# Kernel tuning notes

Hardware: AMD Instinct MI355X
Metric: run time of the kernel (lower is better)

The kernel has to match this reference:

```python
import jax, jax.numpy as jnp
from jax import lax
import numpy as np

B, L, OBS_DIM, ACT_DIM = 4, 1024, 60, 2
D_MODEL, N_LAYERS, D_STATE, D_CONV, EXPAND = 256, 4, 16, 4, 2
D_INNER = EXPAND * D_MODEL
DT_RANK = (D_MODEL + 15) // 16  # mamba_ssm default: ceil(d_model/16)


def setup_inputs() -> dict:
    key = jax.random.key(0)
    ks = jax.random.split(key, 12)
    rn = lambda k, s, sc: jax.random.normal(k, s, jnp.float32) * sc
    return {
        "obs_seq": jax.random.normal(ks[0], (B, L, OBS_DIM), jnp.float32),
        "input_proj_w": rn(ks[1], (D_MODEL, OBS_DIM), OBS_DIM ** -0.5),
        "input_proj_b": jnp.zeros((D_MODEL,), jnp.float32),
        "norm_w": jnp.ones((N_LAYERS, D_MODEL), jnp.float32),
        "norm_b": jnp.zeros((N_LAYERS, D_MODEL), jnp.float32),
        "in_proj_w": rn(ks[2], (N_LAYERS, 2 * D_INNER, D_MODEL), D_MODEL ** -0.5),
        "conv_w": rn(ks[3], (N_LAYERS, D_INNER, D_CONV), D_CONV ** -0.5),
        "conv_b": jnp.zeros((N_LAYERS, D_INNER), jnp.float32),
        "x_proj_w": rn(ks[4], (N_LAYERS, DT_RANK + 2 * D_STATE, D_INNER), D_INNER ** -0.5),
        "dt_proj_w": rn(ks[5], (N_LAYERS, D_INNER, DT_RANK), DT_RANK ** -0.5),
        "dt_proj_b": jnp.full((N_LAYERS, D_INNER), float(np.log(np.expm1(0.01))), jnp.float32),
        "A_log": jnp.log(jnp.broadcast_to(jnp.arange(1, D_STATE + 1, dtype=jnp.float32), (N_LAYERS, D_INNER, D_STATE))),
        "D_skip": jnp.ones((N_LAYERS, D_INNER), jnp.float32),
        "out_proj_w": rn(ks[6], (N_LAYERS, D_MODEL, D_INNER), D_INNER ** -0.5),
        "policy_mean_w": rn(ks[7], (ACT_DIM, D_MODEL), 0.01 * D_MODEL ** -0.5),
        "policy_mean_b": jnp.zeros((ACT_DIM,), jnp.float32),
        "policy_log_std": jnp.zeros((ACT_DIM,), jnp.float32),
        "value_w": rn(ks[8], (1, D_MODEL), D_MODEL ** -0.5),
        "value_b": jnp.zeros((1,), jnp.float32),
    }


def _silu(x):
    return x * jax.nn.sigmoid(x)


def _layer_norm(x, w, b):
    m = jnp.mean(x, -1, keepdims=True)
    v = jnp.mean(jnp.square(x - m), -1, keepdims=True)
    return (x - m) * lax.rsqrt(v + 1e-5) * w + b


def _mamba(x, in_w, cw, cb, xw, dtw, dtb, a_log, d_skip, ow):
    # x: (B, L, d_model)
    xz = jnp.einsum('bld,ed->ble', x, in_w)            # (B, L, 2*d_inner)
    xi, z = xz[..., :D_INNER], xz[..., D_INNER:]
    # depthwise causal conv, width D_CONV
    xp = jnp.pad(xi, ((0, 0), (D_CONV - 1, 0), (0, 0)))
    conv = sum(xp[:, k:k + L, :] * cw[:, k] for k in range(D_CONV)) + cb
    xi = _silu(conv)
    dbc = jnp.einsum('bld,ed->ble', xi, xw)            # (B, L, dt_rank + 2*d_state)
    dt = jax.nn.softplus(jnp.einsum('blr,dr->bld', dbc[..., :DT_RANK], dtw) + dtb)
    Bm = dbc[..., DT_RANK:DT_RANK + D_STATE]           # (B, L, N)
    Cm = dbc[..., DT_RANK + D_STATE:]                  # (B, L, N)
    A = -jnp.exp(a_log)                                # (d_inner, N)
    dA = jnp.exp(dt[..., None] * A)                    # (B, L, d_inner, N)
    dBx = (dt * xi)[..., None] * Bm[:, :, None, :]     # (B, L, d_inner, N)

    def comb(c1, c2):
        a1, b1 = c1
        a2, b2 = c2
        return a2 * a1, a2 * b1 + b2

    _, h = lax.associative_scan(comb, (dA, dBx), axis=1)  # h_t = dA_t*h_{t-1} + dBx_t
    y = jnp.einsum('bldn,bln->bld', h, Cm) + d_skip * xi
    return jnp.einsum('bld,ed->ble', y * _silu(z), ow)


def _forward(obs_seq, input_proj_w, input_proj_b, norm_w, norm_b, in_proj_w, conv_w,
             conv_b, x_proj_w, dt_proj_w, dt_proj_b, A_log, D_skip, out_proj_w,
             policy_mean_w, policy_mean_b, policy_log_std, value_w, value_b):
    x = _silu(jnp.einsum('blo,do->bld', obs_seq, input_proj_w) + input_proj_b)
    for i in range(N_LAYERS):  # pre-norm residual Mamba blocks
        x = x + _mamba(_layer_norm(x, norm_w[i], norm_b[i]), in_proj_w[i], conv_w[i],
                       conv_b[i], x_proj_w[i], dt_proj_w[i], dt_proj_b[i], A_log[i],
                       D_skip[i], out_proj_w[i])
    mu = jnp.einsum('bld,ad->bla', x, policy_mean_w) + policy_mean_b
    std = jnp.broadcast_to(jnp.exp(policy_log_std), mu.shape)
    value = jnp.einsum('bld,od->blo', x, value_w) + value_b
    return mu, std, value


def reference(obs_seq, input_proj_w, input_proj_b, norm_w, norm_b, in_proj_w, conv_w,
              conv_b, x_proj_w, dt_proj_w, dt_proj_b, A_log, D_skip, out_proj_w,
              policy_mean_w, policy_mean_b, policy_log_std, value_w, value_b):
    return _forward(obs_seq, input_proj_w, input_proj_b, norm_w, norm_b, in_proj_w,
                    conv_w, conv_b, x_proj_w, dt_proj_w, dt_proj_b, A_log, D_skip,
                    out_proj_w, policy_mean_w, policy_mean_b, policy_log_std,
                    value_w, value_b)
```

## Files before the change

kernel.cpp:

```cpp
#include <hip/hip_runtime.h>
#include <hip/hip_bf16.h>

#define Bsz 4
#define Lseq 1024
#define OBS 60
#define DM 256
#define DI 512
#define DTR 16
#define DST 16
#define NTOK (Bsz*Lseq)
#define NCH 128
#define CH  8

typedef _Float16 half8 __attribute__((ext_vector_type(8)));
typedef float floatx4 __attribute__((ext_vector_type(4)));

__device__ __forceinline__ float silu_f(float v) {
    return v * (1.f / (1.f + __expf(-v)));
}
__device__ __forceinline__ float softplus_f(float v) {
    return fmaxf(v, 0.f) + log1pf(__expf(-fabsf(v)));
}

__device__ __forceinline__ void compute_dA(float dtv, const float* An,
                                           bool structured, float* dA) {
    if (structured) {
        float p1 = __expf(-dtv);
        float p2 = p1*p1, p4 = p2*p2, p8 = p4*p4;
        dA[0]=p1;      dA[1]=p2;      dA[2]=p2*p1;    dA[3]=p4;
        dA[4]=p4*p1;   dA[5]=p4*p2;   dA[6]=p4*dA[2]; dA[7]=p8;
        dA[8]=p8*p1;   dA[9]=p8*p2;   dA[10]=p8*dA[2];dA[11]=p8*p4;
        dA[12]=p8*dA[4];dA[13]=p8*dA[5];dA[14]=p8*dA[6];dA[15]=p8*p8;
    } else {
        #pragma unroll
        for (int n = 0; n < 16; ++n) dA[n] = __expf(dtv*An[n]);
    }
}

#define NIN_W  (4*1024*256)
#define NX_W   (4*64*512)
#define NOUT_W (4*256*512)
#define NCWT   (4*4*512)
#define NW_TOT (NIN_W + NX_W + NOUT_W + NCWT)
#define NWB    ((NW_TOT + 255)/256)
__global__ __launch_bounds__(256) void prep_kernel(
    const float* __restrict__ inw, const float* __restrict__ xw,
    const float* __restrict__ ow, const float* __restrict__ cw,
    _Float16* __restrict__ wh_in, _Float16* __restrict__ wh_x,
    _Float16* __restrict__ wh_out, _Float16* __restrict__ cwT,
    const float* __restrict__ obs, const float* __restrict__ ipw,
    const float* __restrict__ ipb, const float* __restrict__ nw,
    const float* __restrict__ nb, float* __restrict__ x,
    _Float16* __restrict__ xn_h) {
    __shared__ float so[OBS];
    __shared__ float ps[4];
    __shared__ float mean_s, rstd_s;
    int tid = threadIdx.x;
    if (blockIdx.x < NWB) {
        int idx = blockIdx.x*256 + tid;
        if (idx < NIN_W) {
            wh_in[idx] = (_Float16)inw[idx];
        } else if (idx < NIN_W + NX_W) {
            int r = idx - NIN_W;
            int layer = r >> 15;
            int rem = r & 32767;
            int n = rem >> 9, k = rem & 511;
            wh_x[r] = (_Float16)((n < 48) ? xw[((size_t)layer*48 + n)*512 + k] : 0.f);
        } else if (idx < NIN_W + NX_W + NOUT_W) {
            int r = idx - NIN_W - NX_W;
            wh_out[r] = (_Float16)ow[r];
        } else if (idx < NW_TOT) {
            int r = idx - NIN_W - NX_W - NOUT_W;
            int layer = r >> 11;
            int rem = r & 2047;
            int k = rem >> 9, d = rem & 511;
            cwT[r] = (_Float16)cw[layer*2048 + d*4 + k];
        }
        return;
    }
    int t = blockIdx.x - NWB;
    if (tid < OBS) so[tid] = obs[t*OBS + tid];
    __syncthreads();
    float acc = ipb[tid];
    const float* wr = ipw + tid*OBS;
    #pragma unroll
    for (int k = 0; k < OBS; ++k) acc += so[k]*wr[k];
    float v = silu_f(acc);
    x[t*DM + tid] = v;
    float s = v;
    #pragma unroll
    for (int off = 32; off; off >>= 1) s += __shfl_down(s, off);
    int wid = tid >> 6, lane = tid & 63;
    if (lane == 0) ps[wid] = s;
    __syncthreads();
    if (tid == 0) mean_s = (ps[0]+ps[1]+ps[2]+ps[3]) * (1.f/DM);
    __syncthreads();
    float m = mean_s;
    float d = v - m;
    float sq = d*d;
    #pragma unroll
    for (int off = 32; off; off >>= 1) sq += __shfl_down(sq, off);
    if (lane == 0) ps[wid] = sq;
    __syncthreads();
    if (tid == 0) rstd_s = rsqrtf((ps[0]+ps[1]+ps[2]+ps[3])*(1.f/DM) + 1e-5f);
    __syncthreads();
    xn_h[t*DM + tid] = (_Float16)(d * rstd_s * nw[tid] + nb[tid]);
}

template<int BM, int BN, int WM, int WN, int EPI>
__global__ __launch_bounds__(256) void hgemm_nt(
    const _Float16* __restrict__ A, const _Float16* __restrict__ W,
    void* __restrict__ Cout, const float* __restrict__ resid,
    int M, int N, int K, int ldc,
    const float* __restrict__ e0, const float* __restrict__ e1,
    const float* __restrict__ e2, const float* __restrict__ e3,
    const float* __restrict__ e4,
    float* __restrict__ xout, _Float16* __restrict__ xnh) {
    constexpr int MFR = BM/(WM*16);
    constexpr int NFR = BN/(WN*16);
    __shared__ _Float16 As[BM*64];
    __shared__ _Float16 Bs[BN*64];
    int tid = threadIdx.x;
    int r0 = blockIdx.y*BM, c0 = blockIdx.x*BN;
    int w = tid >> 6, lane = tid & 63;
    int wr = w / WN, wc = w % WN;
    floatx4 acc[MFR][NFR];
    #pragma unroll
    for (int i = 0; i < MFR; ++i)
        #pragma unroll
        for (int j = 0; j < NFR; ++j)
            acc[i][j] = (floatx4)0.f;

    for (int k0 = 0; k0 < K; k0 += 64) {
        #pragma unroll
        for (int c = 0; c < BM/32; ++c) {
            int q = tid + 256*c;
            int row = q >> 3, cc = (q & 7)*8;
            half8 v = *(const half8*)&A[(size_t)(r0 + row)*K + k0 + cc];
            *(half8*)&As[row*64 + (cc ^ ((row & 7) << 3))] = v;
        }
        #pragma unroll
        for (int c = 0; c < BN/32; ++c) {
            int q = tid + 256*c;
            int row = q >> 3, cc = (q & 7)*8;
            half8 v = *(const half8*)&W[(size_t)(c0 + row)*K + k0 + cc];
            *(half8*)&Bs[row*64 + (cc ^ ((row & 7) << 3))] = v;
        }
        __syncthreads();
        #pragma unroll
        for (int kc = 0; kc < 2; ++kc) {
            half8 a[MFR], b[NFR];
            int col = kc*32 + (lane >> 4)*8;
            #pragma unroll
            for (int i = 0; i < MFR; ++i) {
                int row = wr*(BM/WM) + i*16 + (lane & 15);
                a[i] = *(const half8*)&As[row*64 + (col ^ ((row & 7) << 3))];
            }
            #pragma unroll
            for (int j = 0; j < NFR; ++j) {
                int row = wc*(BN/WN) + j*16 + (lane & 15);
                b[j] = *(const half8*)&Bs[row*64 + (col ^ ((row & 7) << 3))];
            }
            #pragma unroll
            for (int i = 0; i < MFR; ++i)
                #pragma unroll
                for (int j = 0; j < NFR; ++j)
                    acc[i][j] = __builtin_amdgcn_mfma_f32_16x16x32_f16(a[i], b[j], acc[i][j], 0, 0, 0);
        }
        __syncthreads();
    }
    if constexpr (EPI == 1) {
        _Float16* C = (_Float16*)Cout;
        #pragma unroll
        for (int i = 0; i < MFR; ++i) {
            int m0 = r0 + wr*(BM/WM) + i*16 + (lane >> 4)*4;
            #pragma unroll
            for (int j = 0; j < NFR; ++j) {
                int col = c0 + wc*(BN/WN) + j*16 + (lane & 15);
                #pragma unroll
                for (int t = 0; t < 4; ++t)
                    C[(size_t)(m0 + t)*ldc + col] = (_Float16)acc[i][j][t];
            }
        }
    } else if constexpr (EPI == 2 || EPI == 3) {
        int g = lane >> 4, ln16 = lane & 15;
        #pragma unroll
        for (int t = 0; t < 4; ++t) {
            int row = r0 + wr*16 + g*4 + t;
            #pragma unroll
            for (int j = 0; j < NFR; ++j)
                acc[0][j][t] += resid[(size_t)row*DM + j*16 + ln16];
        }
        if constexpr (EPI == 2) {
            #pragma unroll
            for (int t = 0; t < 4; ++t) {
                int row = r0 + wr*16 + g*4 + t;
                float s = 0.f, sq = 0.f;
                #pragma unroll
                for (int j = 0; j < NFR; ++j) {
                    float v = acc[0][j][t];
                    xout[(size_t)row*DM + j*16 + ln16] = v;
                    s += v; sq += v*v;
                }
                #pragma unroll
                for (int msk = 1; msk < 16; msk <<= 1) {
                    s += __shfl_xor(s, msk);
                    sq += __shfl_xor(sq, msk);
                }
                float mean = s * (1.f/DM);
                float rstd = rsqrtf(sq*(1.f/DM) - mean*mean + 1e-5f);
                #pragma unroll
                for (int j = 0; j < NFR; ++j) {
                    int col = j*16 + ln16;
                    float v = acc[0][j][t];
                    xnh[(size_t)row*DM + col] =
                        (_Float16)((v - mean)*rstd*e0[col] + e1[col]);
                }
            }
        } else {
            float* out = xout;
            #pragma unroll
            for (int t = 0; t < 4; ++t) {
                int row = r0 + wr*16 + g*4 + t;
                float m0 = 0.f, m1 = 0.f, vv = 0.f;
                #pragma unroll
                for (int j = 0; j < NFR; ++j) {
                    int col = j*16 + ln16;
                    float v = acc[0][j][t];
                    m0 += v*e0[col]; m1 += v*e0[DM + col]; vv += v*e3[col];
                }
                #pragma unroll
                for (int msk = 1; msk < 16; msk <<= 1) {
                    m0 += __shfl_xor(m0, msk);
                    m1 += __shfl_xor(m1, msk);
                    vv += __shfl_xor(vv, msk);
                }
                if (ln16 == 0) {
                    out[row*2 + 0] = m0 + e1[0];
                    out[row*2 + 1] = m1 + e1[1];
                    out[2*NTOK + row*2 + 0] = __expf(e2[0]);
                    out[2*NTOK + row*2 + 1] = __expf(e2[1]);
                    out[4*NTOK + row] = vv + e4[0];
                }
            }
        }
    }
}

__global__ __launch_bounds__(256) void xproj_conv_gemm(
    const _Float16* __restrict__ xz_h, const _Float16* __restrict__ Wx,
    const _Float16* __restrict__ cwT, const float* __restrict__ cb,
    float* __restrict__ dbc) {
    __shared__ _Float16 As[32*64];
    __shared__ _Float16 Bs[64*64];
    int tid = threadIdx.x;
    int r0 = blockIdx.x*32;
    int w = tid >> 6, lane = tid & 63;
    int wr = w >> 1, wc = w & 1;
    floatx4 acc[2];
    acc[0] = (floatx4)0.f; acc[1] = (floatx4)0.f;
    for (int k0 = 0; k0 < 512; k0 += 64) {
        {
            int row = tid >> 3, e8 = tid & 7;
            int d = k0 + e8*8;
            int t = r0 + row, l = t & (Lseq-1);
            half8 zero8 = (half8)((_Float16)0.f);
            half8 v0 = (l >= 3) ? *(const half8*)&xz_h[(size_t)(t-3)*1024 + d] : zero8;
            half8 v1 = (l >= 2) ? *(const half8*)&xz_h[(size_t)(t-2)*1024 + d] : zero8;
            half8 v2 = (l >= 1) ? *(const half8*)&xz_h[(size_t)(t-1)*1024 + d] : zero8;
            half8 v3 = *(const half8*)&xz_h[(size_t)t*1024 + d];
            half8 c0 = *(const half8*)&cwT[0*512 + d];
            half8 c1 = *(const half8*)&cwT[1*512 + d];
            half8 c2 = *(const half8*)&cwT[2*512 + d];
            half8 c3 = *(const half8*)&cwT[3*512 + d];
            half8 o;
            #pragma unroll
            for (int e = 0; e < 8; ++e) {
                float a = cb[d + e];
                a += (float)v0[e]*(float)c0[e];
                a += (float)v1[e]*(float)c1[e];
                a += (float)v2[e]*(float)c2[e];
                a += (float)v3[e]*(float)c3[e];
                o[e] = (_Float16)silu_f(a);
            }
            *(half8*)&As[row*64 + ((e8*8) ^ ((row & 7) << 3))] = o;
        }
        #pragma unroll
        for (int c = 0; c < 2; ++c) {
            int q = tid + 256*c;
            int row = q >> 3, cc = (q & 7)*8;
            half8 vv = *(const half8*)&Wx[(size_t)row*512 + k0 + cc];
            *(half8*)&Bs[row*64 + (cc ^ ((row & 7) << 3))] = vv;
        }
        __syncthreads();
        #pragma unroll
        for (int kc = 0; kc < 2; ++kc) {
            int col = kc*32 + (lane >> 4)*8;
            int arow = wr*16 + (lane & 15);
            half8 a = *(const half8*)&As[arow*64 + (col ^ ((arow & 7) << 3))];
            #pragma unroll
            for (int j = 0; j < 2; ++j) {
                int brow = wc*32 + j*16 + (lane & 15);
                half8 b = *(const half8*)&Bs[brow*64 + (col ^ ((brow & 7) << 3))];
                acc[j] = __builtin_amdgcn_mfma_f32_16x16x32_f16(a, b, acc[j], 0, 0, 0);
            }
        }
        __syncthreads();
    }
    int m0 = r0 + wr*16 + (lane >> 4)*4;
    #pragma unroll
    for (int j = 0; j < 2; ++j) {
        int col = wc*32 + j*16 + (lane & 15);
        if (col < 48) {
            #pragma unroll
            for (int t = 0; t < 4; ++t)
                dbc[(size_t)(m0 + t)*48 + col] = acc[j][t];
        }
    }
}

__global__ __launch_bounds__(256) void scan_phaseA(
    const _Float16* __restrict__ xz_h, const float* __restrict__ dbc,
    const float* __restrict__ dtw, const float* __restrict__ dtb,
    const float* __restrict__ a_log, const float* __restrict__ cw,
    const float* __restrict__ cb,
    _Float16* __restrict__ xi_h, _Float16* __restrict__ dt_h,
    _Float16* __restrict__ Ap, _Float16* __restrict__ He) {
    __shared__ float sdbc[CH*48];
    int blk = blockIdx.x;
    int b = blk >> 8; int rem = blk & 255; int c = rem >> 1; int half = rem & 1;
    int d = half*256 + threadIdx.x;
    const float* src = dbc + ((size_t)(b*Lseq + c*CH))*48;
    for (int q = threadIdx.x; q < CH*48; q += 256) sdbc[q] = src[q];
    float wreg[16];
    #pragma unroll
    for (int r = 0; r < DTR; ++r) wreg[r] = dtw[d*DTR + r];
    float bias = dtb[d];
    float4 cwv = *(const float4*)&cw[d*4];
    float cbv = cb[d];
    float An[16];
    bool structured = true;
    #pragma unroll
    for (int n = 0; n < 16; ++n) {
        An[n] = -__expf(a_log[d*16 + n]);
        structured = structured && (fabsf(An[n] + (float)(n+1)) < 1e-4f*(n+1));
    }
    int l0 = c*CH; int t0 = b*Lseq + l0;
    float w0 = 0.f, w1 = 0.f, w2 = 0.f;
    if (l0 >= 3) {
        w0 = (float)xz_h[(size_t)(t0-3)*1024 + d];
        w1 = (float)xz_h[(size_t)(t0-2)*1024 + d];
        w2 = (float)xz_h[(size_t)(t0-1)*1024 + d];
    }
    __syncthreads();
    float h[16] = {};
    float ap[16];
    #pragma unroll
    for (int n = 0; n < 16; ++n) ap[n] = 1.f;
    #pragma unroll 4
    for (int s = 0; s < CH; ++s) {
        float cur = (float)xz_h[(size_t)(t0+s)*1024 + d];
        float conv = cbv + cwv.x*w0 + cwv.y*w1 + cwv.z*w2 + cwv.w*cur;
        w0 = w1; w1 = w2; w2 = cur;
        float xiv = silu_f(conv);
        float dl = bias;
        #pragma unroll
        for (int r = 0; r < DTR; ++r) dl += sdbc[s*48 + r]*wreg[r];
        float dtv = softplus_f(dl);
        size_t ti = (size_t)(t0+s)*DI + d;
        xi_h[ti] = (_Float16)xiv;
        dt_h[ti] = (_Float16)dtv;
        float u = dtv*xiv;
        float dA[16];
        compute_dA(dtv, An, structured, dA);
        #pragma unroll
        for (int n = 0; n < 16; ++n) {
            h[n] = dA[n]*h[n] + u*sdbc[s*48 + DTR + n];
            ap[n] *= dA[n];
        }
    }
    size_t base = ((size_t)(b*NCH + c)*16)*DI + d;
    #pragma unroll
    for (int n = 0; n < 16; ++n) {
        Ap[base + n*DI] = (_Float16)ap[n];
        He[base + n*DI] = (_Float16)h[n];
    }
}

__global__ __launch_bounds__(256) void scan_phaseB(
    const _Float16* __restrict__ Ap, const _Float16* __restrict__ He,
    _Float16* __restrict__ h0) {
    int g = blockIdx.x*blockDim.x + threadIdx.x;
    int b = g >> 13; int n = (g >> 9) & 15; int d = g & 511;
    float run = 0.f;
    for (int c = 0; c < NCH; ++c) {
        size_t idx = ((size_t)(b*NCH + c)*16 + n)*DI + d;
        float a = (float)Ap[idx], e = (float)He[idx];
        h0[idx] = (_Float16)run;
        run = a*run + e;
    }
}

__global__ __launch_bounds__(256) void scan_phaseC(
    const _Float16* __restrict__ xi_h, const _Float16* __restrict__ dt_h,
    const float* __restrict__ dbc, const float* __restrict__ a_log,
    const float* __restrict__ dskip, const _Float16* __restrict__ xz_h,
    const _Float16* __restrict__ h0, _Float16* __restrict__ yg_h) {
    __shared__ float sdbc[CH*48];
    int blk = blockIdx.x;
    int b = blk >> 8; int rem = blk & 255; int c = rem >> 1; int half = rem & 1;
    int d = half*256 + threadIdx.x;
    const float* src = dbc + ((size_t)(b*Lseq + c*CH))*48;
    for (int q = threadIdx.x; q < CH*48; q += 256) sdbc[q] = src[q];
    float An[16];
    bool structured = true;
    #pragma unroll
    for (int n = 0; n < 16; ++n) {
        An[n] = -__expf(a_log[d*16 + n]);
        structured = structured && (fabsf(An[n] + (float)(n+1)) < 1e-4f*(n+1));
    }
    __syncthreads();
    int t0 = b*Lseq + c*CH;
    float h[16];
    size_t base = ((size_t)(b*NCH + c)*16)*DI + d;
    #pragma unroll
    for (int n = 0; n < 16; ++n) h[n] = (float)h0[base + n*DI];
    float ds = dskip[d];
    #pragma unroll 4
    for (int s = 0; s < CH; ++s) {
        size_t ti = (size_t)(t0+s)*DI + d;
        float xiv = (float)xi_h[ti];
        float dtv = (float)dt_h[ti];
        float u = dtv*xiv;
        float dA[16];
        compute_dA(dtv, An, structured, dA);
        float y = ds*xiv;
        #pragma unroll
        for (int n = 0; n < 16; ++n) {
            h[n] = dA[n]*h[n] + u*sdbc[s*48 + DTR + n];
            y += h[n]*sdbc[s*48 + DTR + DST + n];
        }
        float zv = (float)xz_h[(size_t)(t0+s)*1024 + DI + d];
        yg_h[ti] = (_Float16)(y * silu_f(zv));
    }
}

extern "C" void kernel_launch(void* const* d_in, const int* in_sizes, int n_in,
                              void* d_out, int out_size, void* d_ws, size_t ws_size,
                              hipStream_t stream) {
    const float* obs = (const float*)d_in[0];
    const float* ipw = (const float*)d_in[1];
    const float* ipb = (const float*)d_in[2];
    const float* nw  = (const float*)d_in[3];
    const float* nb  = (const float*)d_in[4];
    const float* inw = (const float*)d_in[5];
    const float* cw  = (const float*)d_in[6];
    const float* cb  = (const float*)d_in[7];
    const float* xw  = (const float*)d_in[8];
    const float* dtw = (const float*)d_in[9];
    const float* dtb = (const float*)d_in[10];
    const float* alog= (const float*)d_in[11];
    const float* dsk = (const float*)d_in[12];
    const float* ow  = (const float*)d_in[13];
    const float* pw  = (const float*)d_in[14];
    const float* pb  = (const float*)d_in[15];
    const float* ls  = (const float*)d_in[16];
    const float* vw  = (const float*)d_in[17];
    const float* vb  = (const float*)d_in[18];
    float* out = (float*)d_out;

    float* ws = (float*)d_ws;
    float* x   = ws;
    float* dbc = x   + 1048576;
    _Float16* f16b  = (_Float16*)(dbc + 196608);
    _Float16* xz_h  = f16b;
    _Float16* xn_h  = xz_h  + 4194304;
    _Float16* xi_h  = xn_h  + 1048576;
    _Float16* dt_h  = xi_h  + 2097152;
    _Float16* yg_h  = dt_h  + 2097152;
    _Float16* Ap_h  = yg_h  + 2097152;
    _Float16* He_h  = Ap_h  + 4194304;
    _Float16* h0_h  = Ap_h;
    _Float16* wh_in = He_h  + 4194304;
    _Float16* wh_x  = wh_in + 1048576;
    _Float16* wh_out= wh_x  + 131072;
    _Float16* cwT_h = wh_out+ 524288;

    prep_kernel<<<NWB + NTOK, 256, 0, stream>>>(
        inw, xw, ow, cw, wh_in, wh_x, wh_out, cwT_h,
        obs, ipw, ipb, nw, nb, x, xn_h);

    for (int i = 0; i < 4; ++i) {
        {
            dim3 g(1024/64, NTOK/128);
            hgemm_nt<128,64,2,2,1><<<g, 256, 0, stream>>>(
                xn_h, wh_in + (size_t)i*1024*256, xz_h, nullptr, NTOK, 1024, 256, 1024,
                nullptr, nullptr, nullptr, nullptr, nullptr, nullptr, nullptr);
        }
        xproj_conv_gemm<<<NTOK/32, 256, 0, stream>>>(
            xz_h, wh_x + (size_t)i*64*512, cwT_h + i*2048, cb + i*DI, dbc);
        scan_phaseA<<<Bsz*NCH*2, 256, 0, stream>>>(
            xz_h, dbc, dtw + (size_t)i*DI*DTR, dtb + i*DI,
            alog + (size_t)i*DI*DST, cw + (size_t)i*DI*4, cb + i*DI,
            xi_h, dt_h, Ap_h, He_h);
        scan_phaseB<<<128, 256, 0, stream>>>(Ap_h, He_h, h0_h);
        scan_phaseC<<<Bsz*NCH*2, 256, 0, stream>>>(
            xi_h, dt_h, dbc, alog + (size_t)i*DI*DST,
            dsk + i*DI, xz_h, h0_h, yg_h);
        {
            dim3 g(1, NTOK/64);
            if (i < 3) {
                hgemm_nt<64,256,4,1,2><<<g, 256, 0, stream>>>(
                    yg_h, wh_out + (size_t)i*256*512, nullptr, x, NTOK, 256, 512, 256,
                    nw + (i+1)*DM, nb + (i+1)*DM, nullptr, nullptr, nullptr, x, xn_h);
            } else {
                hgemm_nt<64,256,4,1,3><<<g, 256, 0, stream>>>(
                    yg_h, wh_out + (size_t)i*256*512, nullptr, x, NTOK, 256, 512, 256,
                    pw, pb, ls, vw, vb, out, nullptr);
            }
        }
    }
}
```

Baseline: 337.3 us.

## Recompute dt in scan phase C and double the scan chunk length

```diff
diff --git a/kernel.cpp b/kernel.cpp
--- a/kernel.cpp
+++ b/kernel.cpp
@@ -9,8 +9,8 @@
 #define DTR 16
 #define DST 16
 #define NTOK (Bsz*Lseq)
-#define NCH 128
-#define CH  8
+#define NCH 64
+#define CH  16
 
 typedef _Float16 half8 __attribute__((ext_vector_type(8)));
 typedef float floatx4 __attribute__((ext_vector_type(4)));
@@ -324,11 +324,11 @@
     const float* __restrict__ dtw, const float* __restrict__ dtb,
     const float* __restrict__ a_log, const float* __restrict__ cw,
     const float* __restrict__ cb,
-    _Float16* __restrict__ xi_h, _Float16* __restrict__ dt_h,
+    _Float16* __restrict__ xi_h,
     _Float16* __restrict__ Ap, _Float16* __restrict__ He) {
     __shared__ float sdbc[CH*48];
     int blk = blockIdx.x;
-    int b = blk >> 8; int rem = blk & 255; int c = rem >> 1; int half = rem & 1;
+    int b = blk >> 7; int rem = blk & 127; int c = rem >> 1; int half = rem & 1;
     int d = half*256 + threadIdx.x;
     const float* src = dbc + ((size_t)(b*Lseq + c*CH))*48;
     for (int q = threadIdx.x; q < CH*48; q += 256) sdbc[q] = src[q];
@@ -357,7 +357,6 @@
     float ap[16];
     #pragma unroll
     for (int n = 0; n < 16; ++n) ap[n] = 1.f;
-    #pragma unroll 4
     for (int s = 0; s < CH; ++s) {
         float cur = (float)xz_h[(size_t)(t0+s)*1024 + d];
         float conv = cbv + cwv.x*w0 + cwv.y*w1 + cwv.z*w2 + cwv.w*cur;
@@ -367,9 +366,7 @@
         #pragma unroll
         for (int r = 0; r < DTR; ++r) dl += sdbc[s*48 + r]*wreg[r];
         float dtv = softplus_f(dl);
-        size_t ti = (size_t)(t0+s)*DI + d;
-        xi_h[ti] = (_Float16)xiv;
-        dt_h[ti] = (_Float16)dtv;
+        xi_h[(size_t)(t0+s)*DI + d] = (_Float16)xiv;
         float u = dtv*xiv;
         float dA[16];
         compute_dA(dtv, An, structured, dA);
@@ -402,16 +399,21 @@
 }
 
 __global__ __launch_bounds__(256) void scan_phaseC(
-    const _Float16* __restrict__ xi_h, const _Float16* __restrict__ dt_h,
-    const float* __restrict__ dbc, const float* __restrict__ a_log,
-    const float* __restrict__ dskip, const _Float16* __restrict__ xz_h,
-    const _Float16* __restrict__ h0, _Float16* __restrict__ yg_h) {
+    const _Float16* __restrict__ xi_h, const float* __restrict__ dbc,
+    const float* __restrict__ dtw, const float* __restrict__ dtb,
+    const float* __restrict__ a_log, const float* __restrict__ dskip,
+    const _Float16* __restrict__ xz_h, const _Float16* __restrict__ h0,
+    _Float16* __restrict__ yg_h) {
     __shared__ float sdbc[CH*48];
     int blk = blockIdx.x;
-    int b = blk >> 8; int rem = blk & 255; int c = rem >> 1; int half = rem & 1;
+    int b = blk >> 7; int rem = blk & 127; int c = rem >> 1; int half = rem & 1;
     int d = half*256 + threadIdx.x;
     const float* src = dbc + ((size_t)(b*Lseq + c*CH))*48;
     for (int q = threadIdx.x; q < CH*48; q += 256) sdbc[q] = src[q];
+    float wreg[16];
+    #pragma unroll
+    for (int r = 0; r < DTR; ++r) wreg[r] = dtw[d*DTR + r];
+    float bias = dtb[d];
     float An[16];
     bool structured = true;
     #pragma unroll
@@ -426,11 +428,13 @@
     #pragma unroll
     for (int n = 0; n < 16; ++n) h[n] = (float)h0[base + n*DI];
     float ds = dskip[d];
-    #pragma unroll 4
     for (int s = 0; s < CH; ++s) {
         size_t ti = (size_t)(t0+s)*DI + d;
         float xiv = (float)xi_h[ti];
-        float dtv = (float)dt_h[ti];
+        float dl = bias;
+        #pragma unroll
+        for (int r = 0; r < DTR; ++r) dl += sdbc[s*48 + r]*wreg[r];
+        float dtv = softplus_f(dl);
         float u = dtv*xiv;
         float dA[16];
         compute_dA(dtv, An, structured, dA);
@@ -476,12 +480,11 @@
     _Float16* xz_h  = f16b;
     _Float16* xn_h  = xz_h  + 4194304;
     _Float16* xi_h  = xn_h  + 1048576;
-    _Float16* dt_h  = xi_h  + 2097152;
-    _Float16* yg_h  = dt_h  + 2097152;
+    _Float16* yg_h  = xi_h  + 2097152;
     _Float16* Ap_h  = yg_h  + 2097152;
-    _Float16* He_h  = Ap_h  + 4194304;
+    _Float16* He_h  = Ap_h  + 2097152;
     _Float16* h0_h  = Ap_h;
-    _Float16* wh_in = He_h  + 4194304;
+    _Float16* wh_in = He_h  + 2097152;
     _Float16* wh_x  = wh_in + 1048576;
     _Float16* wh_out= wh_x  + 131072;
     _Float16* cwT_h = wh_out+ 524288;
@@ -502,11 +505,11 @@
         scan_phaseA<<<Bsz*NCH*2, 256, 0, stream>>>(
             xz_h, dbc, dtw + (size_t)i*DI*DTR, dtb + i*DI,
             alog + (size_t)i*DI*DST, cw + (size_t)i*DI*4, cb + i*DI,
-            xi_h, dt_h, Ap_h, He_h);
+            xi_h, Ap_h, He_h);
         scan_phaseB<<<128, 256, 0, stream>>>(Ap_h, He_h, h0_h);
         scan_phaseC<<<Bsz*NCH*2, 256, 0, stream>>>(
-            xi_h, dt_h, dbc, alog + (size_t)i*DI*DST,
-            dsk + i*DI, xz_h, h0_h, yg_h);
+            xi_h, dbc, dtw + (size_t)i*DI*DTR, dtb + i*DI,
+            alog + (size_t)i*DI*DST, dsk + i*DI, xz_h, h0_h, yg_h);
         {
             dim3 g(1, NTOK/64);
             if (i < 3) {
```

Result: slower. 346.0 us (+2.6%).

## Retile scan chunks and out-proj GEMM, vectorize scan shared-memory loads

Applied to the files above, without the earlier changes.

```diff
diff --git a/kernel.cpp b/kernel.cpp
--- a/kernel.cpp
+++ b/kernel.cpp
@@ -9,8 +9,8 @@
 #define DTR 16
 #define DST 16
 #define NTOK (Bsz*Lseq)
-#define NCH 128
-#define CH  8
+#define NCH 64
+#define CH  16
 
 typedef _Float16 half8 __attribute__((ext_vector_type(8)));
 typedef float floatx4 __attribute__((ext_vector_type(4)));
@@ -107,7 +107,7 @@
     xn_h[t*DM + tid] = (_Float16)(d * rstd_s * nw[tid] + nb[tid]);
 }
 
-template<int BM, int BN, int WM, int WN, int EPI>
+template<int BM, int BN, int WM, int WN, int EPI, int NT = 256>
 __global__ __launch_bounds__(256) void hgemm_nt(
     const _Float16* __restrict__ A, const _Float16* __restrict__ W,
     void* __restrict__ Cout, const float* __restrict__ resid,
@@ -133,15 +133,15 @@
 
     for (int k0 = 0; k0 < K; k0 += 64) {
         #pragma unroll
-        for (int c = 0; c < BM/32; ++c) {
-            int q = tid + 256*c;
+        for (int c = 0; c < BM*8/NT; ++c) {
+            int q = tid + NT*c;
             int row = q >> 3, cc = (q & 7)*8;
             half8 v = *(const half8*)&A[(size_t)(r0 + row)*K + k0 + cc];
             *(half8*)&As[row*64 + (cc ^ ((row & 7) << 3))] = v;
         }
         #pragma unroll
-        for (int c = 0; c < BN/32; ++c) {
-            int q = tid + 256*c;
+        for (int c = 0; c < BN*8/NT; ++c) {
+            int q = tid + NT*c;
             int row = q >> 3, cc = (q & 7)*8;
             half8 v = *(const half8*)&W[(size_t)(c0 + row)*K + k0 + cc];
             *(half8*)&Bs[row*64 + (cc ^ ((row & 7) << 3))] = v;
@@ -326,9 +326,9 @@
     const float* __restrict__ cb,
     _Float16* __restrict__ xi_h, _Float16* __restrict__ dt_h,
     _Float16* __restrict__ Ap, _Float16* __restrict__ He) {
-    __shared__ float sdbc[CH*48];
+    __shared__ __align__(16) float sdbc[CH*48];
     int blk = blockIdx.x;
-    int b = blk >> 8; int rem = blk & 255; int c = rem >> 1; int half = rem & 1;
+    int b = blk >> 7; int rem = blk & 127; int c = rem >> 1; int half = rem & 1;
     int d = half*256 + threadIdx.x;
     const float* src = dbc + ((size_t)(b*Lseq + c*CH))*48;
     for (int q = threadIdx.x; q < CH*48; q += 256) sdbc[q] = src[q];
@@ -357,25 +357,35 @@
     float ap[16];
     #pragma unroll
     for (int n = 0; n < 16; ++n) ap[n] = 1.f;
-    #pragma unroll 4
     for (int s = 0; s < CH; ++s) {
         float cur = (float)xz_h[(size_t)(t0+s)*1024 + d];
         float conv = cbv + cwv.x*w0 + cwv.y*w1 + cwv.z*w2 + cwv.w*cur;
         w0 = w1; w1 = w2; w2 = cur;
         float xiv = silu_f(conv);
-        float dl = bias;
-        #pragma unroll
-        for (int r = 0; r < DTR; ++r) dl += sdbc[s*48 + r]*wreg[r];
-        float dtv = softplus_f(dl);
+        float4 q0 = *(const float4*)&sdbc[s*48 + 0];
+        float4 q1 = *(const float4*)&sdbc[s*48 + 4];
+        float4 q2 = *(const float4*)&sdbc[s*48 + 8];
+        float4 q3 = *(const float4*)&sdbc[s*48 + 12];
+        float dlin = bias
+            + q0.x*wreg[0] + q0.y*wreg[1] + q0.z*wreg[2] + q0.w*wreg[3]
+            + q1.x*wreg[4] + q1.y*wreg[5] + q1.z*wreg[6] + q1.w*wreg[7]
+            + q2.x*wreg[8] + q2.y*wreg[9] + q2.z*wreg[10] + q2.w*wreg[11]
+            + q3.x*wreg[12] + q3.y*wreg[13] + q3.z*wreg[14] + q3.w*wreg[15];
+        float dtv = softplus_f(dlin);
         size_t ti = (size_t)(t0+s)*DI + d;
         xi_h[ti] = (_Float16)xiv;
         dt_h[ti] = (_Float16)dtv;
         float u = dtv*xiv;
         float dA[16];
         compute_dA(dtv, An, structured, dA);
+        float Bv[16];
+        *(float4*)&Bv[0]  = *(const float4*)&sdbc[s*48 + 16];
+        *(float4*)&Bv[4]  = *(const float4*)&sdbc[s*48 + 20];
+        *(float4*)&Bv[8]  = *(const float4*)&sdbc[s*48 + 24];
+        *(float4*)&Bv[12] = *(const float4*)&sdbc[s*48 + 28];
         #pragma unroll
         for (int n = 0; n < 16; ++n) {
-            h[n] = dA[n]*h[n] + u*sdbc[s*48 + DTR + n];
+            h[n] = dA[n]*h[n] + u*Bv[n];
             ap[n] *= dA[n];
         }
     }
@@ -406,9 +416,9 @@
     const float* __restrict__ dbc, const float* __restrict__ a_log,
     const float* __restrict__ dskip, const _Float16* __restrict__ xz_h,
     const _Float16* __restrict__ h0, _Float16* __restrict__ yg_h) {
-    __shared__ float sdbc[CH*48];
+    __shared__ __align__(16) float sdbc[CH*48];
     int blk = blockIdx.x;
-    int b = blk >> 8; int rem = blk & 255; int c = rem >> 1; int half = rem & 1;
+    int b = blk >> 7; int rem = blk & 127; int c = rem >> 1; int half = rem & 1;
     int d = half*256 + threadIdx.x;
     const float* src = dbc + ((size_t)(b*Lseq + c*CH))*48;
     for (int q = threadIdx.x; q < CH*48; q += 256) sdbc[q] = src[q];
@@ -426,7 +436,6 @@
     #pragma unroll
     for (int n = 0; n < 16; ++n) h[n] = (float)h0[base + n*DI];
     float ds = dskip[d];
-    #pragma unroll 4
     for (int s = 0; s < CH; ++s) {
         size_t ti = (size_t)(t0+s)*DI + d;
         float xiv = (float)xi_h[ti];
@@ -434,11 +443,20 @@
         float u = dtv*xiv;
         float dA[16];
         compute_dA(dtv, An, structured, dA);
+        float Bv[16], Cv[16];
+        *(float4*)&Bv[0]  = *(const float4*)&sdbc[s*48 + 16];
+        *(float4*)&Bv[4]  = *(const float4*)&sdbc[s*48 + 20];
+        *(float4*)&Bv[8]  = *(const float4*)&sdbc[s*48 + 24];
+        *(float4*)&Bv[12] = *(const float4*)&sdbc[s*48 + 28];
+        *(float4*)&Cv[0]  = *(const float4*)&sdbc[s*48 + 32];
+        *(float4*)&Cv[4]  = *(const float4*)&sdbc[s*48 + 36];
+        *(float4*)&Cv[8]  = *(const float4*)&sdbc[s*48 + 40];
+        *(float4*)&Cv[12] = *(const float4*)&sdbc[s*48 + 44];
         float y = ds*xiv;
         #pragma unroll
         for (int n = 0; n < 16; ++n) {
-            h[n] = dA[n]*h[n] + u*sdbc[s*48 + DTR + n];
-            y += h[n]*sdbc[s*48 + DTR + DST + n];
+            h[n] = dA[n]*h[n] + u*Bv[n];
+            y += h[n]*Cv[n];
         }
         float zv = (float)xz_h[(size_t)(t0+s)*1024 + DI + d];
         yg_h[ti] = (_Float16)(y * silu_f(zv));
@@ -479,9 +497,9 @@
     _Float16* dt_h  = xi_h  + 2097152;
     _Float16* yg_h  = dt_h  + 2097152;
     _Float16* Ap_h  = yg_h  + 2097152;
-    _Float16* He_h  = Ap_h  + 4194304;
+    _Float16* He_h  = Ap_h  + 2097152;
     _Float16* h0_h  = Ap_h;
-    _Float16* wh_in = He_h  + 4194304;
+    _Float16* wh_in = He_h  + 2097152;
     _Float16* wh_x  = wh_in + 1048576;
     _Float16* wh_out= wh_x  + 131072;
     _Float16* cwT_h = wh_out+ 524288;
@@ -508,13 +526,13 @@
             xi_h, dt_h, dbc, alog + (size_t)i*DI*DST,
             dsk + i*DI, xz_h, h0_h, yg_h);
         {
-            dim3 g(1, NTOK/64);
+            dim3 g(1, NTOK/16);
             if (i < 3) {
-                hgemm_nt<64,256,4,1,2><<<g, 256, 0, stream>>>(
+                hgemm_nt<16,256,1,1,2,64><<<g, 64, 0, stream>>>(
                     yg_h, wh_out + (size_t)i*256*512, nullptr, x, NTOK, 256, 512, 256,
                     nw + (i+1)*DM, nb + (i+1)*DM, nullptr, nullptr, nullptr, x, xn_h);
             } else {
-                hgemm_nt<64,256,4,1,3><<<g, 256, 0, stream>>>(
+                hgemm_nt<16,256,1,1,3,64><<<g, 64, 0, stream>>>(
                     yg_h, wh_out + (size_t)i*256*512, nullptr, x, NTOK, 256, 512, 256,
                     pw, pb, ls, vw, vb, out, nullptr);
             }
```

Measured after the change: 569.9 us. 1.69x slower.
